# Performance work log

Hardware: AMD Instinct MI355X
Metric: run time of the kernel (lower is better)

Reference implementation:

```python
import jax, jax.numpy as jnp
import numpy as np

NUM_HEADS = 16
D_MODEL = 1024
SEQ = 4096
HEAD_DIM = D_MODEL // NUM_HEADS
ROPE_BASE = 10000.0


def _rope(x):
    # x: [h, s, d]  (rotate-half RoPE per head)
    s, d = x.shape[-2], x.shape[-1]
    inv_freq = 1.0 / (ROPE_BASE ** (jnp.arange(0, d, 2, dtype=jnp.float32) / d))  # [d/2]
    ang = jnp.arange(s, dtype=jnp.float32)[:, None] * inv_freq[None, :]           # [s, d/2]
    cos, sin = jnp.cos(ang), jnp.sin(ang)
    x1, x2 = x[..., : d // 2], x[..., d // 2 :]
    return jnp.concatenate([x1 * cos - x2 * sin, x1 * sin + x2 * cos], axis=-1)


def setup_inputs() -> dict:
    key = jax.random.key(0)
    kq, kk, kv, kwq, kwk, kwv = jax.random.split(key, 6)
    scale = 1.0 / np.sqrt(D_MODEL)
    return {
        "q": jax.random.normal(kq, (SEQ, D_MODEL), dtype=jnp.float32),
        "k": jax.random.normal(kk, (SEQ, D_MODEL), dtype=jnp.float32),
        "v": jax.random.normal(kv, (SEQ, D_MODEL), dtype=jnp.float32),
        "mask": jnp.tril(jnp.ones((SEQ, SEQ), dtype=bool)),  # causal
        "Wq": jax.random.normal(kwq, (D_MODEL, D_MODEL), dtype=jnp.float32) * scale,
        "Wk": jax.random.normal(kwk, (D_MODEL, D_MODEL), dtype=jnp.float32) * scale,
        "Wv": jax.random.normal(kwv, (D_MODEL, D_MODEL), dtype=jnp.float32) * scale,
    }


def reference(q, k, v, mask, Wq, Wk, Wv):
    # Projections (eqx Linear: x @ W.T, no bias)
    qp = q @ Wq.T  # [s, d_model]
    kp = k @ Wk.T
    vp = v @ Wv.T
    # split heads: [s, (h d)] -> [h, s, d]
    def split(x):
        return x.reshape(SEQ, NUM_HEADS, HEAD_DIM).transpose(1, 0, 2)
    qh, kh, vh = split(qp), split(kp), split(vp)
    qh = _rope(qh)
    kh = _rope(kh)
    # explicit full logits, masked softmax (matches original, no SDPA)
    logits = jnp.einsum("hqd,hkd->hqk", qh, kh) / jnp.sqrt(jnp.float32(HEAD_DIM))
    logits = jnp.where(mask[None, :, :], logits, -jnp.inf)
    attn = jax.nn.softmax(logits, axis=-1)  # [h, q, k]
    out = jnp.einsum("hqk,hkd->hqd", attn, vh)
    return out.transpose(1, 0, 2).reshape(SEQ, D_MODEL)
```

## Files before the change

kernel.cpp:

```cpp
#include <hip/hip_runtime.h>
#include <math.h>

#define SEQ 4096
#define DMODEL 1024
#define NHEADS 16
#define HDIM 64

typedef __bf16 v8bf __attribute__((ext_vector_type(8)));
typedef float f32x4 __attribute__((ext_vector_type(4)));
typedef float f32x16 __attribute__((ext_vector_type(16)));
typedef int i32x2 __attribute__((ext_vector_type(2)));
typedef int i32x4 __attribute__((ext_vector_type(4)));

#define NPART 4608
#define SCALE_Q 0.18033688011112042f

__device__ __forceinline__ unsigned short f2bf(float f) {
    union { float f; unsigned int u; } v; v.f = f;
    unsigned int u = v.u;
    return (unsigned short)((u + 0x7fffu + ((u >> 16) & 1u)) >> 16);
}

__device__ __forceinline__ int cvtpk(float lo, float hi) {
    int r;
    asm("v_cvt_pk_bf16_f32 %0, %1, %2" : "=v"(r) : "v"(lo), "v"(hi));
    return r;
}

__global__ __launch_bounds__(256) void proj_rope_kernel(
    const float* __restrict__ Xq, const float* __restrict__ Xk, const float* __restrict__ Xv,
    const float* __restrict__ Wq, const float* __restrict__ Wk, const float* __restrict__ Wv,
    unsigned short* __restrict__ qh, unsigned short* __restrict__ kh,
    unsigned short* __restrict__ vht)
{
    const int tz = blockIdx.z;
    const float* __restrict__ X = (tz == 0) ? Xq : (tz == 1) ? Xk : Xv;
    const float* __restrict__ W = (tz == 0) ? Wq : (tz == 1) ? Wk : Wv;

    const int tid = threadIdx.x;
    const int lane = tid & 63;
    const int wid = tid >> 6;
    const int l15 = lane & 15;
    const int l4 = lane >> 4;
    const int wr = wid >> 1, wc = wid & 1;

    const int m0 = blockIdx.x * 128;
    const int n0 = blockIdx.y * 128;

    __shared__ __align__(16) unsigned short Ab[2][128 * 32];
    __shared__ __align__(16) unsigned short Bb[2][128 * 32];

    int srow[4], sc4[4], sbyte[4];
    #pragma unroll
    for (int c = 0; c < 4; ++c) {
        int i = tid + (c << 8);
        int row = i >> 3;
        int c4 = (i & 7) << 2;
        srow[c] = row; sc4[c] = c4;
        sbyte[c] = row * 64 + (((c4 >> 3) ^ ((row >> 1) & 3)) << 4) + ((c4 << 1) & 15);
    }

    float4 ra[4], rb[4];

    auto GLOAD = [&](int kt) {
        const int k0 = kt << 5;
        #pragma unroll
        for (int c = 0; c < 4; ++c) {
            ra[c] = *reinterpret_cast<const float4*>(X + (size_t)(m0 + srow[c]) * DMODEL + k0 + sc4[c]);
            rb[c] = *reinterpret_cast<const float4*>(W + (size_t)(n0 + srow[c]) * DMODEL + k0 + sc4[c]);
        }
    };
    auto PACKW = [&](int b) {
        #pragma unroll
        for (int c = 0; c < 4; ++c) {
            uint2 pa, pb;
            pa.x = (unsigned)cvtpk(ra[c].x, ra[c].y);
            pa.y = (unsigned)cvtpk(ra[c].z, ra[c].w);
            pb.x = (unsigned)cvtpk(rb[c].x, rb[c].y);
            pb.y = (unsigned)cvtpk(rb[c].z, rb[c].w);
            *reinterpret_cast<uint2*>(reinterpret_cast<char*>(Ab[b]) + sbyte[c]) = pa;
            *reinterpret_cast<uint2*>(reinterpret_cast<char*>(Bb[b]) + sbyte[c]) = pb;
        }
    };

    f32x4 acc[4][4] = {};

    GLOAD(0);
    PACKW(0);

    for (int kt = 0; kt < 32; ++kt) {
        __syncthreads();
        const bool hn = (kt < 31);
        if (hn) GLOAD(kt + 1);

        const unsigned short* A = Ab[kt & 1];
        const unsigned short* B = Bb[kt & 1];

        v8bf af[4], bfr[4];
        #pragma unroll
        for (int mi = 0; mi < 4; ++mi) {
            int row = wr * 64 + mi * 16 + l15;
            int byte = row * 64 + ((l4 ^ ((row >> 1) & 3)) << 4);
            af[mi] = *reinterpret_cast<const v8bf*>(reinterpret_cast<const char*>(A) + byte);
        }
        #pragma unroll
        for (int ni = 0; ni < 4; ++ni) {
            int row = wc * 64 + ni * 16 + l15;
            int byte = row * 64 + ((l4 ^ ((row >> 1) & 3)) << 4);
            bfr[ni] = *reinterpret_cast<const v8bf*>(reinterpret_cast<const char*>(B) + byte);
        }
        #pragma unroll
        for (int mi = 0; mi < 4; ++mi)
            #pragma unroll
            for (int ni = 0; ni < 4; ++ni)
                acc[mi][ni] = __builtin_amdgcn_mfma_f32_16x16x32_bf16(af[mi], bfr[ni], acc[mi][ni], 0, 0, 0);

        if (hn) PACKW((kt + 1) & 1);
    }

    const int h = (n0 >> 6) + wc;
    const int mbase = m0 + wr * 64;
    if (tz == 2) {
        unsigned short* base = vht + (size_t)h * HDIM * SEQ;
        #pragma unroll
        for (int mi = 0; mi < 4; ++mi) {
            #pragma unroll
            for (int ni = 0; ni < 4; ++ni) {
                int d = ni * 16 + l15;
                int m = mbase + mi * 16 + l4 * 4;
                uint2 pk;
                pk.x = (unsigned)cvtpk(acc[mi][ni][0], acc[mi][ni][1]);
                pk.y = (unsigned)cvtpk(acc[mi][ni][2], acc[mi][ni][3]);
                *reinterpret_cast<uint2*>(base + (size_t)d * SEQ + m) = pk;
            }
        }
    } else {
        unsigned short* base = ((tz == 0) ? qh : kh) + (size_t)h * SEQ * HDIM;
        const float scl = (tz == 0) ? SCALE_Q : 1.0f;
        #pragma unroll
        for (int ni = 0; ni < 2; ++ni) {
            int j = ni * 16 + l15;
            float invf = expf(-(float)j * 0.28782313662425574f);
            #pragma unroll
            for (int mi = 0; mi < 4; ++mi) {
                #pragma unroll
                for (int r = 0; r < 4; ++r) {
                    int m = mbase + mi * 16 + l4 * 4 + r;
                    float ang = (float)m * invf;
                    float sn, cs;
                    sincosf(ang, &sn, &cs);
                    sn *= scl; cs *= scl;
                    float x1 = acc[mi][ni][r];
                    float x2 = acc[mi][ni + 2][r];
                    base[(size_t)m * HDIM + j]      = f2bf(x1 * cs - x2 * sn);
                    base[(size_t)m * HDIM + j + 32] = f2bf(x1 * sn + x2 * cs);
                }
            }
        }
    }
}

__global__ __launch_bounds__(256) void repack_kernel(
    const unsigned short* __restrict__ kh, const unsigned short* __restrict__ vht,
    unsigned short* __restrict__ kfr, unsigned short* __restrict__ vfr)
{
    const int lane = threadIdx.x & 63;
    const int wid = threadIdx.x >> 6;
    const int l31 = lane & 31;
    const int l5 = lane >> 5;
    const int h = blockIdx.x >> 4;
    const int T = ((blockIdx.x & 15) << 2) + wid;

    const unsigned short* __restrict__ ksrc = kh + ((size_t)h * SEQ + T * 64) * HDIM;
    unsigned short* __restrict__ kdst = kfr + ((size_t)(h * 64 + T)) * 4096 + lane * 8;
    #pragma unroll
    for (int ns = 0; ns < 2; ++ns)
        #pragma unroll
        for (int dk = 0; dk < 4; ++dk) {
            v8bf f = *reinterpret_cast<const v8bf*>(ksrc + (ns * 32 + l31) * HDIM + dk * 16 + l5 * 8);
            *reinterpret_cast<v8bf*>(kdst + (ns * 4 + dk) * 512) = f;
        }

    const unsigned short* __restrict__ vsrc = vht + ((size_t)h * 64) * SEQ;
    unsigned short* __restrict__ vdst = vfr + ((size_t)(h * 64 + T)) * 4096 + lane * 8;
    #pragma unroll
    for (int dt = 0; dt < 2; ++dt)
        #pragma unroll
        for (int kb = 0; kb < 4; ++kb) {
            v8bf f = *reinterpret_cast<const v8bf*>(
                vsrc + (size_t)(dt * 32 + l31) * SEQ + T * 64 + kb * 16 + l5 * 8);
            *reinterpret_cast<v8bf*>(vdst + (dt * 4 + kb) * 512) = f;
        }
}

__global__ __launch_bounds__(64, 2) void attn_kernel(
    const unsigned short* __restrict__ qh, const unsigned short* __restrict__ kfr,
    const unsigned short* __restrict__ vfr, float* __restrict__ out,
    unsigned short* __restrict__ po, float* __restrict__ ml)
{
    const int lane = threadIdx.x & 63;
    const int l31 = lane & 31;
    const int l5 = lane >> 5;

    const int bid = blockIdx.x;
    const int xcd = bid & 7;
    const int idx = bid >> 3;
    const int hsel = (idx >= 320) ? 1 : 0;
    const int h = (xcd << 1) | hsel;
    const int r = 319 - (idx - hsel * 320);

    int qb, c, nc;
    if (r < 32)       { qb = r;                     c = 0;            nc = 1; }
    else if (r < 96)  { qb = 32 + ((r - 32) >> 1);  c = (r - 32) & 1; nc = 2; }
    else if (r < 192) { int rr = r - 96; qb = 64 + rr / 3; c = rr - (qb - 64) * 3; nc = 3; }
    else              { int rr = r - 192; qb = 96 + (rr >> 2); c = rr & 3; nc = 4; }

    const int q0 = qb * 32;
    const int q = q0 + l31;
    const int nt = (q0 + 32 + 63) >> 6;
    const int t0 = c * 16;
    const int t1 = min(t0 + 16, nt);

    const unsigned short* __restrict__ qbase = qh + ((size_t)h * SEQ + q) * HDIM + l5 * 8;
    const unsigned short* __restrict__ kfh = kfr + (size_t)h * 262144 + lane * 8;
    const unsigned short* __restrict__ vfh = vfr + (size_t)h * 262144 + lane * 8;

    v8bf qf[4];
    #pragma unroll
    for (int dk = 0; dk < 4; ++dk)
        qf[dk] = *reinterpret_cast<const v8bf*>(qbase + dk * 16);

    f32x16 of[2] = {};
    float mreg = -INFINITY, lreg = 0.0f;

    auto LOADK = [&](v8bf (&KB)[8], int T) {
        const unsigned short* kp = kfh + (size_t)T * 4096;
        #pragma unroll
        for (int f = 0; f < 8; ++f)
            KB[f] = *reinterpret_cast<const v8bf*>(kp + f * 512);
    };

    auto ROUND = [&](int T, v8bf (&KC)[8], v8bf (&KN)[8]) {
        v8bf vf[8];
        {
            const unsigned short* vp = vfh + (size_t)T * 4096;
            #pragma unroll
            for (int f = 0; f < 8; ++f)
                vf[f] = *reinterpret_cast<const v8bf*>(vp + f * 512);
        }
        if (T + 1 < t1) LOADK(KN, T + 1);

        f32x16 st[2];
        __builtin_amdgcn_s_setprio(1);
        #pragma unroll
        for (int ns = 0; ns < 2; ++ns) {
            f32x16 acc = {};
            #pragma unroll
            for (int dk = 0; dk < 4; ++dk)
                acc = __builtin_amdgcn_mfma_f32_32x32x16_bf16(KC[ns * 4 + dk], qf[dk], acc, 0, 0, 0);
            st[ns] = acc;
        }
        __builtin_amdgcn_s_setprio(0);

        if (T == nt - 1) {
            const int kvb = T * 64 + 4 * l5;
            #pragma unroll
            for (int ns = 0; ns < 2; ++ns)
                #pragma unroll
                for (int i = 0; i < 16; ++i) {
                    int kv = kvb + ns * 32 + (i & 3) + 8 * (i >> 2);
                    if (kv > q) st[ns][i] = -INFINITY;
                }
        }

        float t16[16];
        #pragma unroll
        for (int i = 0; i < 16; ++i) t16[i] = fmaxf(st[0][i], st[1][i]);
        #pragma unroll
        for (int i = 0; i < 8; ++i) t16[i] = fmaxf(t16[i], t16[i + 8]);
        #pragma unroll
        for (int i = 0; i < 4; ++i) t16[i] = fmaxf(t16[i], t16[i + 4]);
        float pmax = fmaxf(fmaxf(t16[0], t16[1]), fmaxf(t16[2], t16[3]));
        {
            i32x2 sw = __builtin_amdgcn_permlane32_swap(__float_as_int(pmax), __float_as_int(pmax), false, false);
            pmax = fmaxf(__int_as_float(sw.x), __int_as_float(sw.y));
        }

        if (!__all(pmax - mreg <= 8.0f)) {
            float mnew = fmaxf(mreg, pmax);
            float sc = exp2f(mreg - mnew);
            lreg *= sc;
            #pragma unroll
            for (int dt = 0; dt < 2; ++dt)
                #pragma unroll
                for (int i = 0; i < 16; ++i) of[dt][i] *= sc;
            mreg = mnew;
        }

        float ps0 = 0.f, ps1 = 0.f, ps2 = 0.f, ps3 = 0.f;
        #pragma unroll
        for (int ns = 0; ns < 2; ++ns)
            #pragma unroll
            for (int i = 0; i < 16; ++i) {
                float p = exp2f(st[ns][i] - mreg);
                st[ns][i] = p;
                if ((i & 3) == 0) ps0 += p; else if ((i & 3) == 1) ps1 += p;
                else if ((i & 3) == 2) ps2 += p; else ps3 += p;
            }
        lreg += (ps0 + ps1) + (ps2 + ps3);

        v8bf pt[4];
        #pragma unroll
        for (int kb = 0; kb < 4; ++kb) {
            int ns = kb >> 1, kp = (kb & 1) * 8;
            int A0 = cvtpk(st[ns][kp + 0], st[ns][kp + 1]);
            int A1 = cvtpk(st[ns][kp + 2], st[ns][kp + 3]);
            int B0 = cvtpk(st[ns][kp + 4], st[ns][kp + 5]);
            int B1 = cvtpk(st[ns][kp + 6], st[ns][kp + 7]);
            i32x2 s0 = __builtin_amdgcn_permlane32_swap(A0, B0, false, false);
            i32x2 s1 = __builtin_amdgcn_permlane32_swap(A1, B1, false, false);
            i32x4 u; u.x = s0.x; u.y = s1.x; u.z = s0.y; u.w = s1.y;
            v8bf p; __builtin_memcpy(&p, &u, 16);
            pt[kb] = p;
        }

        __builtin_amdgcn_s_setprio(1);
        #pragma unroll
        for (int dt = 0; dt < 2; ++dt)
            #pragma unroll
            for (int kb = 0; kb < 4; ++kb)
                of[dt] = __builtin_amdgcn_mfma_f32_32x32x16_bf16(vf[dt * 4 + kb], pt[kb], of[dt], 0, 0, 0);
        __builtin_amdgcn_s_setprio(0);
    };

    v8bf kA[8], kB[8];
    LOADK(kA, t0);
    int t = t0;
    while (true) {
        ROUND(t, kA, kB);
        if (++t == t1) break;
        ROUND(t, kB, kA);
        if (++t == t1) break;
    }

    {
        i32x2 sw = __builtin_amdgcn_permlane32_swap(__float_as_int(lreg), __float_as_int(lreg), false, false);
        lreg = __int_as_float(sw.x) + __int_as_float(sw.y);
    }

    if (nc == 1) {
        float inv = 1.0f / lreg;
        float* obase = out + (size_t)q * DMODEL + h * HDIM + l5 * 4;
        #pragma unroll
        for (int dt = 0; dt < 2; ++dt)
            #pragma unroll
            for (int g = 0; g < 4; ++g) {
                f32x4 o4;
                o4[0] = of[dt][g * 4 + 0] * inv;
                o4[1] = of[dt][g * 4 + 1] * inv;
                o4[2] = of[dt][g * 4 + 2] * inv;
                o4[3] = of[dt][g * 4 + 3] * inv;
                *reinterpret_cast<f32x4*>(obase + dt * 32 + g * 8) = o4;
            }
    } else {
        const int p = h * 288 + (r - 32);
        unsigned short* pb = po + ((size_t)p * 32 + l31) * 64 + l5 * 4;
        #pragma unroll
        for (int dt = 0; dt < 2; ++dt)
            #pragma unroll
            for (int g = 0; g < 4; ++g) {
                uint2 u;
                u.x = (unsigned)cvtpk(of[dt][g * 4 + 0], of[dt][g * 4 + 1]);
                u.y = (unsigned)cvtpk(of[dt][g * 4 + 2], of[dt][g * 4 + 3]);
                *reinterpret_cast<uint2*>(pb + dt * 32 + g * 8) = u;
            }
        if (l5 == 0) {
            float2 v; v.x = mreg; v.y = lreg;
            reinterpret_cast<float2*>(ml)[(size_t)p * 32 + l31] = v;
        }
    }
}

__global__ __launch_bounds__(256) void combine_kernel(
    const unsigned short* __restrict__ po, const float* __restrict__ ml,
    float* __restrict__ out)
{
    const int b = blockIdx.x;
    const int h = b / 96;
    const int j = b - h * 96;
    const int qb = 32 + j;
    int nc, r0;
    if (qb < 64)      { nc = 2; r0 = 32 + ((qb - 32) << 1); }
    else if (qb < 96) { nc = 3; r0 = 96 + (qb - 64) * 3; }
    else              { nc = 4; r0 = 192 + ((qb - 96) << 2); }
    const int p0 = h * 288 + (r0 - 32);
    const int d = threadIdx.x & 63;
    const int rg = threadIdx.x >> 6;
    const int q0 = qb * 32;

    for (int row = rg; row < 32; row += 4) {
        float mc[4], lc[4];
        float M = -INFINITY;
        #pragma unroll
        for (int ci = 0; ci < 4; ++ci)
            if (ci < nc) {
                float2 v = reinterpret_cast<const float2*>(ml)[(size_t)(p0 + ci) * 32 + row];
                mc[ci] = v.x; lc[ci] = v.y;
                M = fmaxf(M, v.x);
            }
        float L = 0.0f, O = 0.0f;
        #pragma unroll
        for (int ci = 0; ci < 4; ++ci)
            if (ci < nc) {
                float w = exp2f(mc[ci] - M);
                L += lc[ci] * w;
                unsigned int raw = po[((size_t)(p0 + ci) * 32 + row) * 64 + d];
                union { unsigned int u; float f; } cv; cv.u = raw << 16;
                O += cv.f * w;
            }
        out[(size_t)(q0 + row) * DMODEL + h * HDIM + d] = O / L;
    }
}

extern "C" void kernel_launch(void* const* d_in, const int* in_sizes, int n_in,
                              void* d_out, int out_size, void* d_ws, size_t ws_size,
                              hipStream_t stream) {
    (void)in_sizes; (void)n_in; (void)out_size; (void)ws_size;
    const float* q  = (const float*)d_in[0];
    const float* k  = (const float*)d_in[1];
    const float* v  = (const float*)d_in[2];
    const float* Wq = (const float*)d_in[4];
    const float* Wk = (const float*)d_in[5];
    const float* Wv = (const float*)d_in[6];

    unsigned short* qh  = (unsigned short*)d_ws;
    unsigned short* kfr = qh  + (size_t)NHEADS * SEQ * HDIM;
    unsigned short* vfr = kfr + (size_t)NHEADS * SEQ * HDIM;
    unsigned short* kh  = vfr + (size_t)NHEADS * SEQ * HDIM;
    unsigned short* vht = kh  + (size_t)NHEADS * SEQ * HDIM;
    unsigned short* po  = kh;
    float* ml = (float*)(po + (size_t)NPART * 32 * 64);
    float* out = (float*)d_out;

    dim3 g1(SEQ / 128, DMODEL / 128, 3);
    proj_rope_kernel<<<g1, 256, 0, stream>>>(q, k, v, Wq, Wk, Wv, qh, kh, vht);

    repack_kernel<<<dim3(256), 256, 0, stream>>>(kh, vht, kfr, vfr);

    attn_kernel<<<dim3(16 * 320), 64, 0, stream>>>(qh, kfr, vfr, out, po, ml);

    combine_kernel<<<dim3(16 * 96), 256, 0, stream>>>(po, ml, out);
}
```

Baseline: 161.5 us.

## Pre-cast inputs to bf16, stage GEMM via direct LDS loads, fuse repack

```diff
diff --git a/kernel.cpp b/kernel.cpp
--- a/kernel.cpp
+++ b/kernel.cpp
@@ -27,15 +27,44 @@
     return r;
 }
 
+__device__ __forceinline__ void gload16(const unsigned short* g, unsigned short* l) {
+    __builtin_amdgcn_global_load_lds(
+        (const __attribute__((address_space(1))) unsigned int*)g,
+        (__attribute__((address_space(3))) unsigned int*)l, 16, 0, 0);
+}
+
+__global__ __launch_bounds__(256) void cast_kernel(
+    const float* __restrict__ q, const float* __restrict__ k, const float* __restrict__ v,
+    const float* __restrict__ wq, const float* __restrict__ wk, const float* __restrict__ wv,
+    unsigned short* __restrict__ xq, unsigned short* __restrict__ xk,
+    unsigned short* __restrict__ xv, unsigned short* __restrict__ wb)
+{
+    const size_t M4 = (size_t)4 << 20, M1 = (size_t)1 << 20;
+    size_t i = ((size_t)blockIdx.x * 256 + threadIdx.x) * 8;
+    const float* s; unsigned short* d; size_t off;
+    if (i < M4)                 { s = q;  d = xq;          off = i; }
+    else if (i < 2 * M4)        { s = k;  d = xk;          off = i - M4; }
+    else if (i < 3 * M4)        { s = v;  d = xv;          off = i - 2 * M4; }
+    else if (i < 3 * M4 + M1)   { s = wq; d = wb;          off = i - 3 * M4; }
+    else if (i < 3 * M4 + 2*M1) { s = wk; d = wb + M1;     off = i - 3 * M4 - M1; }
+    else                        { s = wv; d = wb + 2 * M1; off = i - 3 * M4 - 2 * M1; }
+    float4 a = *reinterpret_cast<const float4*>(s + off);
+    float4 b = *reinterpret_cast<const float4*>(s + off + 4);
+    uint4 u;
+    u.x = (unsigned)cvtpk(a.x, a.y); u.y = (unsigned)cvtpk(a.z, a.w);
+    u.z = (unsigned)cvtpk(b.x, b.y); u.w = (unsigned)cvtpk(b.z, b.w);
+    *reinterpret_cast<uint4*>(d + off) = u;
+}
+
 __global__ __launch_bounds__(256) void proj_rope_kernel(
-    const float* __restrict__ Xq, const float* __restrict__ Xk, const float* __restrict__ Xv,
-    const float* __restrict__ Wq, const float* __restrict__ Wk, const float* __restrict__ Wv,
-    unsigned short* __restrict__ qh, unsigned short* __restrict__ kh,
-    unsigned short* __restrict__ vht)
+    const unsigned short* __restrict__ Xq, const unsigned short* __restrict__ Xk,
+    const unsigned short* __restrict__ Xv, const unsigned short* __restrict__ Wb,
+    unsigned short* __restrict__ qh, unsigned short* __restrict__ kfr,
+    unsigned short* __restrict__ vfr)
 {
     const int tz = blockIdx.z;
-    const float* __restrict__ X = (tz == 0) ? Xq : (tz == 1) ? Xk : Xv;
-    const float* __restrict__ W = (tz == 0) ? Wq : (tz == 1) ? Wk : Wv;
+    const unsigned short* __restrict__ X = (tz == 0) ? Xq : (tz == 1) ? Xk : Xv;
+    const unsigned short* __restrict__ W = Wb + (size_t)tz * ((size_t)1 << 20);
 
     const int tid = threadIdx.x;
     const int lane = tid & 63;
@@ -47,51 +76,34 @@
     const int m0 = blockIdx.x * 128;
     const int n0 = blockIdx.y * 128;
 
-    __shared__ __align__(16) unsigned short Ab[2][128 * 32];
-    __shared__ __align__(16) unsigned short Bb[2][128 * 32];
-
-    int srow[4], sc4[4], sbyte[4];
+    __shared__ __align__(16) unsigned short Ab[2][4096];
+    __shared__ __align__(16) unsigned short Bb[2][4096];
+
+    int grow[2], gcol[2];
     #pragma unroll
-    for (int c = 0; c < 4; ++c) {
-        int i = tid + (c << 8);
-        int row = i >> 3;
-        int c4 = (i & 7) << 2;
-        srow[c] = row; sc4[c] = c4;
-        sbyte[c] = row * 64 + (((c4 >> 3) ^ ((row >> 1) & 3)) << 4) + ((c4 << 1) & 15);
-    }
-
-    float4 ra[4], rb[4];
-
-    auto GLOAD = [&](int kt) {
+    for (int g = 0; g < 2; ++g) {
+        int row = wid * 32 + g * 16 + (lane >> 2);
+        grow[g] = row;
+        gcol[g] = 8 * ((lane & 3) ^ ((row >> 1) & 3));
+    }
+
+    auto STAGE = [&](int b, int kt) {
         const int k0 = kt << 5;
         #pragma unroll
-        for (int c = 0; c < 4; ++c) {
-            ra[c] = *reinterpret_cast<const float4*>(X + (size_t)(m0 + srow[c]) * DMODEL + k0 + sc4[c]);
-            rb[c] = *reinterpret_cast<const float4*>(W + (size_t)(n0 + srow[c]) * DMODEL + k0 + sc4[c]);
+        for (int g = 0; g < 2; ++g) {
+            gload16(X + (size_t)(m0 + grow[g]) * DMODEL + k0 + gcol[g],
+                    &Ab[b][(wid * 2 + g) * 512]);
+            gload16(W + (size_t)(n0 + grow[g]) * DMODEL + k0 + gcol[g],
+                    &Bb[b][(wid * 2 + g) * 512]);
         }
     };
-    auto PACKW = [&](int b) {
-        #pragma unroll
-        for (int c = 0; c < 4; ++c) {
-            uint2 pa, pb;
-            pa.x = (unsigned)cvtpk(ra[c].x, ra[c].y);
-            pa.y = (unsigned)cvtpk(ra[c].z, ra[c].w);
-            pb.x = (unsigned)cvtpk(rb[c].x, rb[c].y);
-            pb.y = (unsigned)cvtpk(rb[c].z, rb[c].w);
-            *reinterpret_cast<uint2*>(reinterpret_cast<char*>(Ab[b]) + sbyte[c]) = pa;
-            *reinterpret_cast<uint2*>(reinterpret_cast<char*>(Bb[b]) + sbyte[c]) = pb;
-        }
-    };
 
     f32x4 acc[4][4] = {};
 
-    GLOAD(0);
-    PACKW(0);
-
+    STAGE(0, 0);
     for (int kt = 0; kt < 32; ++kt) {
         __syncthreads();
-        const bool hn = (kt < 31);
-        if (hn) GLOAD(kt + 1);
+        if (kt < 31) STAGE((kt + 1) & 1, kt + 1);
 
         const unsigned short* A = Ab[kt & 1];
         const unsigned short* B = Bb[kt & 1];
@@ -114,29 +126,28 @@
             #pragma unroll
             for (int ni = 0; ni < 4; ++ni)
                 acc[mi][ni] = __builtin_amdgcn_mfma_f32_16x16x32_bf16(af[mi], bfr[ni], acc[mi][ni], 0, 0, 0);
-
-        if (hn) PACKW((kt + 1) & 1);
     }
 
     const int h = (n0 >> 6) + wc;
     const int mbase = m0 + wr * 64;
+    const int T = blockIdx.x * 2 + wr;
+
     if (tz == 2) {
-        unsigned short* base = vht + (size_t)h * HDIM * SEQ;
+        unsigned short* vb = vfr + (size_t)h * 262144 + (size_t)T * 4096;
         #pragma unroll
         for (int mi = 0; mi < 4; ++mi) {
             #pragma unroll
             for (int ni = 0; ni < 4; ++ni) {
-                int d = ni * 16 + l15;
-                int m = mbase + mi * 16 + l4 * 4;
+                int f = (ni >> 1) * 4 + mi;
+                int off = f * 512 + ((l4 >> 1) * 32 + (ni & 1) * 16 + l15) * 8 + (l4 & 1) * 4;
                 uint2 pk;
                 pk.x = (unsigned)cvtpk(acc[mi][ni][0], acc[mi][ni][1]);
                 pk.y = (unsigned)cvtpk(acc[mi][ni][2], acc[mi][ni][3]);
-                *reinterpret_cast<uint2*>(base + (size_t)d * SEQ + m) = pk;
-            }
-        }
-    } else {
-        unsigned short* base = ((tz == 0) ? qh : kh) + (size_t)h * SEQ * HDIM;
-        const float scl = (tz == 0) ? SCALE_Q : 1.0f;
+                *reinterpret_cast<uint2*>(vb + off) = pk;
+            }
+        }
+    } else if (tz == 1) {
+        unsigned short* kb = kfr + (size_t)h * 262144 + (size_t)T * 4096;
         #pragma unroll
         for (int ni = 0; ni < 2; ++ni) {
             int j = ni * 16 + l15;
@@ -149,7 +160,30 @@
                     float ang = (float)m * invf;
                     float sn, cs;
                     sincosf(ang, &sn, &cs);
-                    sn *= scl; cs *= scl;
+                    float x1 = acc[mi][ni][r];
+                    float x2 = acc[mi][ni + 2][r];
+                    int rowoff = ((l15 >> 3) * 32 + (mi & 1) * 16 + l4 * 4 + r) * 8 + (l15 & 7);
+                    int fb = (mi >> 1) * 4;
+                    kb[(fb + ni) * 512 + rowoff]     = f2bf(x1 * cs - x2 * sn);
+                    kb[(fb + ni + 2) * 512 + rowoff] = f2bf(x1 * sn + x2 * cs);
+                }
+            }
+        }
+    } else {
+        unsigned short* base = qh + (size_t)h * SEQ * HDIM;
+        #pragma unroll
+        for (int ni = 0; ni < 2; ++ni) {
+            int j = ni * 16 + l15;
+            float invf = expf(-(float)j * 0.28782313662425574f);
+            #pragma unroll
+            for (int mi = 0; mi < 4; ++mi) {
+                #pragma unroll
+                for (int r = 0; r < 4; ++r) {
+                    int m = mbase + mi * 16 + l4 * 4 + r;
+                    float ang = (float)m * invf;
+                    float sn, cs;
+                    sincosf(ang, &sn, &cs);
+                    sn *= SCALE_Q; cs *= SCALE_Q;
                     float x1 = acc[mi][ni][r];
                     float x2 = acc[mi][ni + 2][r];
                     base[(size_t)m * HDIM + j]      = f2bf(x1 * cs - x2 * sn);
@@ -158,39 +192,6 @@
             }
         }
     }
-}
-
-__global__ __launch_bounds__(256) void repack_kernel(
-    const unsigned short* __restrict__ kh, const unsigned short* __restrict__ vht,
-    unsigned short* __restrict__ kfr, unsigned short* __restrict__ vfr)
-{
-    const int lane = threadIdx.x & 63;
-    const int wid = threadIdx.x >> 6;
-    const int l31 = lane & 31;
-    const int l5 = lane >> 5;
-    const int h = blockIdx.x >> 4;
-    const int T = ((blockIdx.x & 15) << 2) + wid;
-
-    const unsigned short* __restrict__ ksrc = kh + ((size_t)h * SEQ + T * 64) * HDIM;
-    unsigned short* __restrict__ kdst = kfr + ((size_t)(h * 64 + T)) * 4096 + lane * 8;
-    #pragma unroll
-    for (int ns = 0; ns < 2; ++ns)
-        #pragma unroll
-        for (int dk = 0; dk < 4; ++dk) {
-            v8bf f = *reinterpret_cast<const v8bf*>(ksrc + (ns * 32 + l31) * HDIM + dk * 16 + l5 * 8);
-            *reinterpret_cast<v8bf*>(kdst + (ns * 4 + dk) * 512) = f;
-        }
-
-    const unsigned short* __restrict__ vsrc = vht + ((size_t)h * 64) * SEQ;
-    unsigned short* __restrict__ vdst = vfr + ((size_t)(h * 64 + T)) * 4096 + lane * 8;
-    #pragma unroll
-    for (int dt = 0; dt < 2; ++dt)
-        #pragma unroll
-        for (int kb = 0; kb < 4; ++kb) {
-            v8bf f = *reinterpret_cast<const v8bf*>(
-                vsrc + (size_t)(dt * 32 + l31) * SEQ + T * 64 + kb * 16 + l5 * 8);
-            *reinterpret_cast<v8bf*>(vdst + (dt * 4 + kb) * 512) = f;
-        }
 }
 
 __global__ __launch_bounds__(64, 2) void attn_kernel(
@@ -433,19 +434,23 @@
     const float* Wk = (const float*)d_in[5];
     const float* Wv = (const float*)d_in[6];
 
+    const size_t M4 = (size_t)4 << 20;
     unsigned short* qh  = (unsigned short*)d_ws;
-    unsigned short* kfr = qh  + (size_t)NHEADS * SEQ * HDIM;
-    unsigned short* vfr = kfr + (size_t)NHEADS * SEQ * HDIM;
-    unsigned short* kh  = vfr + (size_t)NHEADS * SEQ * HDIM;
-    unsigned short* vht = kh  + (size_t)NHEADS * SEQ * HDIM;
-    unsigned short* po  = kh;
+    unsigned short* kfr = qh  + M4;
+    unsigned short* vfr = kfr + M4;
+    unsigned short* scratch = vfr + M4;
+    unsigned short* Xbv = scratch;
+    unsigned short* Wb  = scratch + M4;
+    unsigned short* po  = scratch;
     float* ml = (float*)(po + (size_t)NPART * 32 * 64);
+    unsigned short* Xbq = (unsigned short*)d_out;
+    unsigned short* Xbk = Xbq + M4;
     float* out = (float*)d_out;
 
+    cast_kernel<<<dim3(7680), 256, 0, stream>>>(q, k, v, Wq, Wk, Wv, Xbq, Xbk, Xbv, Wb);
+
     dim3 g1(SEQ / 128, DMODEL / 128, 3);
-    proj_rope_kernel<<<g1, 256, 0, stream>>>(q, k, v, Wq, Wk, Wv, qh, kh, vht);
-
-    repack_kernel<<<dim3(256), 256, 0, stream>>>(kh, vht, kfr, vfr);
+    proj_rope_kernel<<<g1, 256, 0, stream>>>(Xbq, Xbk, Xbv, Wb, qh, kfr, vfr);
 
     attn_kernel<<<dim3(16 * 320), 64, 0, stream>>>(qh, kfr, vfr, out, po, ml);
 
```

Result: no change. 164.2 us (+1.6%).
